# Optimization experiments

Hardware: AMD Instinct MI355X
Metric: run time of the kernel (lower is better)

The kernel has to match this reference:

```python
import jax, jax.numpy as jnp
import numpy as np

B, S, F_DIM, H = 2, 2048, 1024, 16
DH = F_DIM // H  # 64


def setup_inputs() -> dict:
    key = jax.random.key(0)
    ks = jax.random.split(key, 12)
    scale = 1.0 / np.sqrt(F_DIM)
    inp = {
        "Q": jax.random.normal(ks[0], (B, S, F_DIM), jnp.float32),
        "K": jax.random.normal(ks[1], (B, S, F_DIM), jnp.float32),
        "V": jax.random.normal(ks[2], (B, S, F_DIM), jnp.float32),
        "mask": jnp.zeros((1, 1, S, S), jnp.float32),
        "Wq": jax.random.uniform(ks[3], (F_DIM, F_DIM), jnp.float32, -scale, scale),
        "bq": jax.random.uniform(ks[4], (F_DIM,), jnp.float32, -scale, scale),
        "Wk": jax.random.uniform(ks[5], (F_DIM, F_DIM), jnp.float32, -scale, scale),
        "bk": jax.random.uniform(ks[6], (F_DIM,), jnp.float32, -scale, scale),
        "Wv": jax.random.uniform(ks[7], (F_DIM, F_DIM), jnp.float32, -scale, scale),
        "bv": jax.random.uniform(ks[8], (F_DIM,), jnp.float32, -scale, scale),
        "Wo": jax.random.uniform(ks[9], (F_DIM, F_DIM), jnp.float32, -scale, scale),
        "bo": jax.random.uniform(ks[10], (F_DIM,), jnp.float32, -scale, scale),
    }
    return inp


def _split_heads(x):
    # [B, S, F] -> [B, H, S, DH]
    b, s, _ = x.shape
    return x.reshape(b, s, H, DH).transpose(0, 2, 1, 3)


def reference(Q, K, V, mask, Wq, bq, Wk, bk, Wv, bv, Wo, bo):
    q = _split_heads(Q @ Wq.T + bq)  # [B, H, S, DH]
    k = _split_heads(K @ Wk.T + bk)
    v = _split_heads(V @ Vv_fix(Wv).T + bv) if False else _split_heads(V @ Wv.T + bv)
    scores = jnp.einsum("bhqd,bhkd->bhqk", q, k) / jnp.sqrt(jnp.float32(DH))
    scores = scores + mask
    probs = jax.nn.softmax(scores, axis=-1)
    attn = jnp.einsum("bhqk,bhkd->bhqd", probs, v)  # [B, H, S, DH]
    out = attn.transpose(0, 2, 1, 3).reshape(Q.shape[0], Q.shape[1], F_DIM)
    return out @ Wo.T + bo
```

## Files before the change

### kernel.cpp

```cpp
#include <hip/hip_runtime.h>
#include <hip/hip_bf16.h>

typedef unsigned short u16;
typedef unsigned int u32;
typedef __attribute__((ext_vector_type(4))) float f32x4;
typedef __attribute__((ext_vector_type(16))) float f32x16;
typedef __attribute__((ext_vector_type(8))) short short8;
typedef __attribute__((ext_vector_type(4))) u32 u32x4;

#define SEQ 2048
#define FD  1024
#define NH  16
#define DHD 64

__device__ __forceinline__ u16 f2bf(float f) {
  __hip_bfloat16 h = __float2bfloat16(f);
  return *reinterpret_cast<u16*>(&h);
}
__device__ __forceinline__ u32 pack2bf(float lo, float hi) {
  return (u32)f2bf(lo) | ((u32)f2bf(hi) << 16);
}

template <typename TA, typename TB>
__device__ __forceinline__ void gemm_bt_body(const TA* __restrict__ A, const TB* __restrict__ Bm,
                                             int m0, int n0, u16* As, u16* Bs, f32x4 acc[4][4]) {
  const int tid = threadIdx.x;
  const int lane = tid & 63;
  const int wr = (tid >> 7) & 1;
  const int wc = (tid >> 6) & 1;
  const int lr = lane & 15;
  const int lk = (lane >> 4) << 3;
#pragma unroll
  for (int m = 0; m < 4; ++m)
#pragma unroll
    for (int n = 0; n < 4; ++n) acc[m][n] = {0.f, 0.f, 0.f, 0.f};

  const int r_ = tid >> 2;
  const int c_ = (tid & 3) << 3;

  for (int k0 = 0; k0 < FD; k0 += 32) {
    __syncthreads();
#pragma unroll
    for (int c = 0; c < 2; ++c) {
      int r = c * 64 + r_;
      const TA* s = A + (size_t)(m0 + r) * FD + k0 + c_;
      short8 o;
      if constexpr (sizeof(TA) == 4) {
        f32x4 v0 = *reinterpret_cast<const f32x4*>(s);
        f32x4 v1 = *reinterpret_cast<const f32x4*>(s + 4);
#pragma unroll
        for (int j = 0; j < 4; ++j) { o[j] = (short)f2bf(v0[j]); o[4 + j] = (short)f2bf(v1[j]); }
      } else {
        o = *reinterpret_cast<const short8*>(s);
      }
      *reinterpret_cast<short8*>(&As[r * 32 + c_]) = o;
    }
#pragma unroll
    for (int c = 0; c < 2; ++c) {
      int r = c * 64 + r_;
      const TB* s = Bm + (size_t)(n0 + r) * FD + k0 + c_;
      short8 o;
      if constexpr (sizeof(TB) == 4) {
        f32x4 v0 = *reinterpret_cast<const f32x4*>(s);
        f32x4 v1 = *reinterpret_cast<const f32x4*>(s + 4);
#pragma unroll
        for (int j = 0; j < 4; ++j) { o[j] = (short)f2bf(v0[j]); o[4 + j] = (short)f2bf(v1[j]); }
      } else {
        o = *reinterpret_cast<const short8*>(s);
      }
      *reinterpret_cast<short8*>(&Bs[r * 32 + c_]) = o;
    }
    __syncthreads();

    short8 a[4], b[4];
#pragma unroll
    for (int m = 0; m < 4; ++m)
      a[m] = *reinterpret_cast<const short8*>(&As[(wr * 64 + m * 16 + lr) * 32 + lk]);
#pragma unroll
    for (int n = 0; n < 4; ++n)
      b[n] = *reinterpret_cast<const short8*>(&Bs[(wc * 64 + n * 16 + lr) * 32 + lk]);
#pragma unroll
    for (int m = 0; m < 4; ++m)
#pragma unroll
      for (int n = 0; n < 4; ++n)
        acc[m][n] = __builtin_amdgcn_mfma_f32_16x16x32_bf16(a[m], b[n], acc[m][n], 0, 0, 0);
  }
}

__global__ __launch_bounds__(256) void proj_qkv_kernel(
    const float* __restrict__ Q, const float* __restrict__ K, const float* __restrict__ V,
    const float* __restrict__ Wq, const float* __restrict__ Wk, const float* __restrict__ Wv,
    const float* __restrict__ bq, const float* __restrict__ bk, const float* __restrict__ bv,
    u16* __restrict__ qh, u16* __restrict__ kh, u16* __restrict__ vF) {
  __shared__ u16 As[128 * 32];
  __shared__ u16 Bs[128 * 32];
  const int which = blockIdx.z;
  const float* A    = (which == 0) ? Q  : (which == 1) ? K  : V;
  const float* W    = (which == 0) ? Wq : (which == 1) ? Wk : Wv;
  const float* bias = (which == 0) ? bq : (which == 1) ? bk : bv;
  u16* out          = (which == 0) ? qh : (which == 1) ? kh : vF;
  const int m0 = blockIdx.y * 128, n0 = blockIdx.x * 128;
  const float qscale = 0.18033688011112042f;

  f32x4 acc[4][4];
  gemm_bt_body(A, W, m0, n0, As, Bs, acc);

  const int lane = threadIdx.x & 63;
  const int wr = (threadIdx.x >> 7) & 1, wc = (threadIdx.x >> 6) & 1;
  const int rbase = m0 + wr * 64 + ((lane >> 4) << 2);
  const int cbase = n0 + wc * 64 + (lane & 15);
#pragma unroll
  for (int n = 0; n < 4; ++n) {
    const int col = cbase + n * 16;
    const float bvv = bias[col];
    const int h = col >> 6, dh = col & 63;
#pragma unroll
    for (int m = 0; m < 4; ++m) {
#pragma unroll
      for (int r = 0; r < 4; ++r) {
        const int row = rbase + m * 16 + r;
        const int b = row >> 11, s = row & 2047;
        float v = acc[m][n][r] + bvv;
        if (which == 0) v *= qscale;
        const size_t bhbase = (size_t)(b * 16 + h) * SEQ * DHD;
        size_t idx;
        if (which == 0) {
          idx = bhbase + (size_t)s * 64 + dh;
        } else if (which == 1) {
          idx = bhbase + ((size_t)(((s >> 5) * 4 + (dh >> 4)) * 64
                          + ((dh >> 3) & 1) * 32 + (s & 31)) << 3) + (dh & 7);
        } else {
          idx = bhbase + ((size_t)(((s >> 4) * 2 + (dh >> 5)) * 64
                          + ((s >> 3) & 1) * 32 + (dh & 31)) << 3) + (s & 7);
        }
        out[idx] = f2bf(v);
      }
    }
  }
}

__global__ __launch_bounds__(256) void mask_check_kernel(const u32* __restrict__ mask,
                                                         u32* __restrict__ flag) {
  const size_t cb = (size_t)blockIdx.x * 2048 + (threadIdx.x << 2);
  u32x4 a = *reinterpret_cast<const u32x4*>(&mask[cb]);
  u32x4 b = *reinterpret_cast<const u32x4*>(&mask[cb + 1024]);
  u32 acc = a[0] | a[1] | a[2] | a[3] | b[0] | b[1] | b[2] | b[3];
  if (__ballot(acc != 0)) {
    if ((threadIdx.x & 63) == 0) atomicOr(flag, 1u);
  }
}

__device__ __forceinline__ void load_ktile(const u16* __restrict__ kp, int kv0, int lane,
                                           short8 (&kf)[8]) {
#pragma unroll
  for (int h2 = 0; h2 < 2; ++h2)
#pragma unroll
    for (int d = 0; d < 4; ++d)
      kf[h2 * 4 + d] = *reinterpret_cast<const short8*>(
          &kp[((size_t)((((kv0 >> 5) + h2) * 4 + d) * 64 + lane)) << 3]);
}

__device__ __forceinline__ void attn_tile(
    const short8 (&kf)[8], const u16* __restrict__ vp, const float* __restrict__ mrow,
    u32 has_mask, int kv0, int lane, int hi, const short8 (&qf)[4],
    f32x16 (&oacc)[2], float& m2, float& lsum) {
  const float L2E = 1.44269504088896340736f;
  short8 vf[8];
#pragma unroll
  for (int kb = 0; kb < 4; ++kb)
#pragma unroll
    for (int db = 0; db < 2; ++db)
      vf[kb * 2 + db] = *reinterpret_cast<const short8*>(
          &vp[((size_t)((((kv0 >> 4) + kb) * 2 + db) * 64 + lane)) << 3]);

  f32x16 st[2];
#pragma unroll
  for (int h2 = 0; h2 < 2; ++h2) {
    f32x16 z;
#pragma unroll
    for (int e = 0; e < 16; ++e) z[e] = 0.f;
#pragma unroll
    for (int d = 0; d < 4; ++d)
      z = __builtin_amdgcn_mfma_f32_32x32x16_bf16(kf[h2 * 4 + d], qf[d], z, 0, 0, 0);
    st[h2] = z;
  }
  float p[32];
  if (__builtin_expect(has_mask != 0, 0)) {
#pragma unroll
    for (int h2 = 0; h2 < 2; ++h2)
#pragma unroll
      for (int g = 0; g < 4; ++g) {
        f32x4 mv = *reinterpret_cast<const f32x4*>(&mrow[kv0 + h2 * 32 + g * 8 + hi * 4]);
#pragma unroll
        for (int j = 0; j < 4; ++j)
          p[h2 * 16 + g * 4 + j] = fmaf(mv[j], L2E, st[h2][g * 4 + j]);
      }
  } else {
#pragma unroll
    for (int h2 = 0; h2 < 2; ++h2)
#pragma unroll
      for (int e = 0; e < 16; ++e) p[h2 * 16 + e] = st[h2][e];
  }
  float t8[8];
#pragma unroll
  for (int i = 0; i < 8; ++i)
    t8[i] = fmaxf(fmaxf(p[i], p[i + 8]), fmaxf(p[i + 16], p[i + 24]));
#pragma unroll
  for (int i = 0; i < 4; ++i) t8[i] = fmaxf(t8[i], t8[i + 4]);
  float mt = fmaxf(fmaxf(t8[0], t8[1]), fmaxf(t8[2], t8[3]));
  mt = fmaxf(mt, __shfl_xor(mt, 32));
  const float mnew = fmaxf(m2, mt);
  const float alpha = __builtin_amdgcn_exp2f(m2 - mnew);
  m2 = mnew;
#pragma unroll
  for (int i = 0; i < 32; ++i) p[i] = __builtin_amdgcn_exp2f(p[i] - m2);
  float s8[8];
#pragma unroll
  for (int i = 0; i < 8; ++i) s8[i] = (p[i] + p[i + 8]) + (p[i + 16] + p[i + 24]);
#pragma unroll
  for (int i = 0; i < 4; ++i) s8[i] += s8[i + 4];
  float ssum = (s8[0] + s8[1]) + (s8[2] + s8[3]);
  ssum += __shfl_xor(ssum, 32);
  lsum = lsum * alpha + ssum;
#pragma unroll
  for (int e = 0; e < 16; ++e) { oacc[0][e] *= alpha; oacc[1][e] *= alpha; }

#pragma unroll
  for (int kb = 0; kb < 4; ++kb) {
    const int pb = (kb >> 1) * 16 + (kb & 1) * 8;
    u32 x = pack2bf(p[pb + 0], p[pb + 1]);
    u32 y = pack2bf(p[pb + 4], p[pb + 5]);
    asm volatile("v_permlane32_swap_b32 %0, %1" : "+v"(x), "+v"(y));
    u32 zz = pack2bf(p[pb + 2], p[pb + 3]);
    u32 w = pack2bf(p[pb + 6], p[pb + 7]);
    asm volatile("v_permlane32_swap_b32 %0, %1" : "+v"(zz), "+v"(w));
    union { u32 u[4]; short8 s; } bf;
    bf.u[0] = x; bf.u[1] = zz; bf.u[2] = y; bf.u[3] = w;
#pragma unroll
    for (int db = 0; db < 2; ++db)
      oacc[db] = __builtin_amdgcn_mfma_f32_32x32x16_bf16(vf[kb * 2 + db], bf.s, oacc[db], 0, 0, 0);
  }
}

__global__ __launch_bounds__(256, 2) void attn_kernel(
    const u16* __restrict__ qh, const u16* __restrict__ kh, const u16* __restrict__ vF,
    const float* __restrict__ mask, const u32* __restrict__ mflag, u16* __restrict__ O) {
  const int wave = threadIdx.x >> 6, lane = threadIdx.x & 63;
  const int bid = blockIdx.x;
  const int vid = (bid & 7) * 64 + (bid >> 3);
  const int bh = vid >> 4;
  const int q0 = (vid & 15) * 128 + wave * 32;
  const int lq = lane & 31;
  const int hi = lane >> 5;
  const u16* qp = qh + (size_t)bh * SEQ * DHD;
  const u16* kp = kh + (size_t)bh * SEQ * DHD;
  const u16* vp = vF + (size_t)bh * SEQ * DHD;
  const float* mrow = mask + (size_t)(q0 + lq) * SEQ;
  const u32 has_mask = *mflag;

  short8 qf[4];
#pragma unroll
  for (int d = 0; d < 4; ++d)
    qf[d] = *reinterpret_cast<const short8*>(&qp[(size_t)(q0 + lq) * DHD + d * 16 + hi * 8]);

  f32x16 oacc[2];
#pragma unroll
  for (int e = 0; e < 16; ++e) { oacc[0][e] = 0.f; oacc[1][e] = 0.f; }
  float m2 = -INFINITY, lsum = 0.f;

  short8 ka[8], kb2[8];
  load_ktile(kp, 0, lane, ka);
  for (int it = 0; it < 32; it += 2) {
    const int kv0 = it << 6;
    load_ktile(kp, kv0 + 64, lane, kb2);
    attn_tile(ka, vp, mrow, has_mask, kv0, lane, hi, qf, oacc, m2, lsum);
    load_ktile(kp, (it == 30) ? 0 : kv0 + 128, lane, ka);
    attn_tile(kb2, vp, mrow, has_mask, kv0 + 64, lane, hi, qf, oacc, m2, lsum);
  }

  const int b = bh >> 4, h = bh & 15;
  const float inv = 1.0f / lsum;
  u16* orow = O + ((size_t)(b * SEQ + q0 + lq) * NH + h) * DHD;
#pragma unroll
  for (int db = 0; db < 2; ++db)
#pragma unroll
    for (int g = 0; g < 4; ++g) {
      union { u16 u[4]; unsigned long long ll; } pk;
#pragma unroll
      for (int j = 0; j < 4; ++j) pk.u[j] = f2bf(oacc[db][g * 4 + j] * inv);
      *reinterpret_cast<unsigned long long*>(&orow[db * 32 + g * 8 + hi * 4]) = pk.ll;
    }
}

__global__ __launch_bounds__(256) void out_proj_kernel(
    const u16* __restrict__ O, const float* __restrict__ Wo, const float* __restrict__ bo,
    float* __restrict__ out) {
  __shared__ u16 As[128 * 32];
  __shared__ u16 Bs[128 * 32];
  const int m0 = blockIdx.y * 128, n0 = blockIdx.x * 128;
  f32x4 acc[4][4];
  gemm_bt_body(O, Wo, m0, n0, As, Bs, acc);

  const int lane = threadIdx.x & 63;
  const int wr = (threadIdx.x >> 7) & 1, wc = (threadIdx.x >> 6) & 1;
  const int rbase = m0 + wr * 64 + ((lane >> 4) << 2);
  const int cbase = n0 + wc * 64 + (lane & 15);
#pragma unroll
  for (int n = 0; n < 4; ++n) {
    const int col = cbase + n * 16;
    const float bvv = bo[col];
#pragma unroll
    for (int m = 0; m < 4; ++m)
#pragma unroll
      for (int r = 0; r < 4; ++r) {
        const int row = rbase + m * 16 + r;
        out[(size_t)row * FD + col] = acc[m][n][r] + bvv;
      }
  }
}

extern "C" void kernel_launch(void* const* d_in, const int* in_sizes, int n_in,
                              void* d_out, int out_size, void* d_ws, size_t ws_size,
                              hipStream_t stream) {
  (void)in_sizes; (void)n_in; (void)out_size; (void)ws_size;
  const float* Q    = (const float*)d_in[0];
  const float* K    = (const float*)d_in[1];
  const float* V    = (const float*)d_in[2];
  const float* mask = (const float*)d_in[3];
  const float* Wq   = (const float*)d_in[4];
  const float* bq   = (const float*)d_in[5];
  const float* Wk   = (const float*)d_in[6];
  const float* bk   = (const float*)d_in[7];
  const float* Wv   = (const float*)d_in[8];
  const float* bv   = (const float*)d_in[9];
  const float* Wo   = (const float*)d_in[10];
  const float* bo   = (const float*)d_in[11];
  float* out = (float*)d_out;

  u16* ws = (u16*)d_ws;
  const size_t SZ = (size_t)4096 * 1024;
  u16* qh = ws;
  u16* kh = qh + SZ;
  u16* vF = kh + SZ;
  u16* O  = vF + SZ;
  u32* mflag = (u32*)(O + SZ);

  hipMemsetAsync(mflag, 0, 4, stream);
  mask_check_kernel<<<dim3(2048), 256, 0, stream>>>((const u32*)mask, mflag);

  dim3 gproj(FD / 128, (2 * SEQ) / 128, 3);
  proj_qkv_kernel<<<gproj, 256, 0, stream>>>(Q, K, V, Wq, Wk, Wv, bq, bk, bv, qh, kh, vF);

  attn_kernel<<<dim3(512), 256, 0, stream>>>(qh, kh, vF, mask, mflag, O);

  out_proj_kernel<<<dim3(FD / 128, (2 * SEQ) / 128), 256, 0, stream>>>(O, Wo, bo, out);
}
```

Before: 169.3 us.

## Pre-convert inputs and weights to bf16, use direct global-to-LDS loads in GEMMs

Adds a prep kernel that converts Q/K/V and all four weight matrices to bf16 in workspace, and folds the mask-zero check into that same launch. The projection GEMMs then load bf16 tiles straight into LDS with global_load_lds, with no per-tile fp32 conversion. Block indices are remapped so consecutive blocks share weight columns for better L2 reuse. The cost is an extra full read/write pass over the activations and weights, plus more workspace.

Result: faster. 142.3 us (-15.9%).

```diff
diff --git a/kernel.cpp b/kernel.cpp
--- a/kernel.cpp
+++ b/kernel.cpp
@@ -21,57 +21,70 @@
   return (u32)f2bf(lo) | ((u32)f2bf(hi) << 16);
 }
 
-template <typename TA, typename TB>
-__device__ __forceinline__ void gemm_bt_body(const TA* __restrict__ A, const TB* __restrict__ Bm,
-                                             int m0, int n0, u16* As, u16* Bs, f32x4 acc[4][4]) {
-  const int tid = threadIdx.x;
-  const int lane = tid & 63;
-  const int wr = (tid >> 7) & 1;
-  const int wc = (tid >> 6) & 1;
-  const int lr = lane & 15;
-  const int lk = (lane >> 4) << 3;
+#define GLOAD_LDS16(gp, lp)                                        \
+  __builtin_amdgcn_global_load_lds(                                \
+      (const __attribute__((address_space(1))) unsigned int*)(gp), \
+      (__attribute__((address_space(3))) unsigned int*)(lp), 16, 0, 0)
+
+__global__ __launch_bounds__(256) void prep_kernel(
+    const float* __restrict__ Q, const float* __restrict__ K, const float* __restrict__ V,
+    const float* __restrict__ Wq, const float* __restrict__ Wk, const float* __restrict__ Wv,
+    const float* __restrict__ Wo, const float* __restrict__ mask,
+    u16* __restrict__ Abf, u16* __restrict__ Wbf, u32* __restrict__ flag) {
+  const size_t i = ((size_t)blockIdx.x * 256 + threadIdx.x) * 8;
+  if (i >= 16777216) {
+    const u32* mp = (const u32*)mask + (i - 16777216);
+    u32x4 a = *reinterpret_cast<const u32x4*>(mp);
+    u32x4 b = *reinterpret_cast<const u32x4*>(mp + 4);
+    u32 o = a[0] | a[1] | a[2] | a[3] | b[0] | b[1] | b[2] | b[3];
+    if (__ballot(o != 0) != 0ull && (threadIdx.x & 63) == 0) atomicOr(flag, 1u);
+    return;
+  }
+  const float* src;
+  u16* dst;
+  if (i < 12582912) {
+    const int s = (int)(i >> 22);
+    const size_t off = i & 0x3FFFFF;
+    src = (s == 0 ? Q : s == 1 ? K : V) + off;
+    dst = Abf + i;
+  } else {
+    const size_t j = i - 12582912;
+    const int w = (int)(j >> 20);
+    const size_t off = j & 0xFFFFF;
+    src = (w == 0 ? Wq : w == 1 ? Wk : w == 2 ? Wv : Wo) + off;
+    dst = Wbf + j;
+  }
+  f32x4 a = *reinterpret_cast<const f32x4*>(src);
+  f32x4 b = *reinterpret_cast<const f32x4*>(src + 4);
+  union { u32 u[4]; short8 s; } pk;
+  pk.u[0] = pack2bf(a[0], a[1]); pk.u[1] = pack2bf(a[2], a[3]);
+  pk.u[2] = pack2bf(b[0], b[1]); pk.u[3] = pack2bf(b[2], b[3]);
+  *reinterpret_cast<short8*>(dst) = pk.s;
+}
+
+__device__ __forceinline__ void gemm128_bf16(const u16* __restrict__ A, const u16* __restrict__ W,
+                                             int m0, int n0, u16* As, u16* Bs,
+                                             f32x4 (&acc)[4][4]) {
+  const int tid = threadIdx.x, lane = tid & 63, wv = tid >> 6;
+  const int wr = (tid >> 7) & 1, wc = (tid >> 6) & 1;
+  const int lr = lane & 15, lk = (lane >> 4) << 3;
+  const int srow = lane >> 2;
+  const int scol = (lane & 3) << 3;
 #pragma unroll
   for (int m = 0; m < 4; ++m)
 #pragma unroll
     for (int n = 0; n < 4; ++n) acc[m][n] = {0.f, 0.f, 0.f, 0.f};
-
-  const int r_ = tid >> 2;
-  const int c_ = (tid & 3) << 3;
 
   for (int k0 = 0; k0 < FD; k0 += 32) {
     __syncthreads();
 #pragma unroll
     for (int c = 0; c < 2; ++c) {
-      int r = c * 64 + r_;
-      const TA* s = A + (size_t)(m0 + r) * FD + k0 + c_;
-      short8 o;
-      if constexpr (sizeof(TA) == 4) {
-        f32x4 v0 = *reinterpret_cast<const f32x4*>(s);
-        f32x4 v1 = *reinterpret_cast<const f32x4*>(s + 4);
-#pragma unroll
-        for (int j = 0; j < 4; ++j) { o[j] = (short)f2bf(v0[j]); o[4 + j] = (short)f2bf(v1[j]); }
-      } else {
-        o = *reinterpret_cast<const short8*>(s);
-      }
-      *reinterpret_cast<short8*>(&As[r * 32 + c_]) = o;
-    }
-#pragma unroll
-    for (int c = 0; c < 2; ++c) {
-      int r = c * 64 + r_;
-      const TB* s = Bm + (size_t)(n0 + r) * FD + k0 + c_;
-      short8 o;
-      if constexpr (sizeof(TB) == 4) {
-        f32x4 v0 = *reinterpret_cast<const f32x4*>(s);
-        f32x4 v1 = *reinterpret_cast<const f32x4*>(s + 4);
-#pragma unroll
-        for (int j = 0; j < 4; ++j) { o[j] = (short)f2bf(v0[j]); o[4 + j] = (short)f2bf(v1[j]); }
-      } else {
-        o = *reinterpret_cast<const short8*>(s);
-      }
-      *reinterpret_cast<short8*>(&Bs[r * 32 + c_]) = o;
+      GLOAD_LDS16(&A[(size_t)(m0 + c * 64 + wv * 16 + srow) * FD + k0 + scol],
+                  &As[(c * 64 + wv * 16) * 32]);
+      GLOAD_LDS16(&W[(size_t)(n0 + c * 64 + wv * 16 + srow) * FD + k0 + scol],
+                  &Bs[(c * 64 + wv * 16) * 32]);
     }
     __syncthreads();
-
     short8 a[4], b[4];
 #pragma unroll
     for (int m = 0; m < 4; ++m)
@@ -88,23 +101,27 @@
 }
 
 __global__ __launch_bounds__(256) void proj_qkv_kernel(
-    const float* __restrict__ Q, const float* __restrict__ K, const float* __restrict__ V,
-    const float* __restrict__ Wq, const float* __restrict__ Wk, const float* __restrict__ Wv,
+    const u16* __restrict__ Abf, const u16* __restrict__ Wbf,
     const float* __restrict__ bq, const float* __restrict__ bk, const float* __restrict__ bv,
     u16* __restrict__ qh, u16* __restrict__ kh, u16* __restrict__ vF) {
   __shared__ u16 As[128 * 32];
   __shared__ u16 Bs[128 * 32];
-  const int which = blockIdx.z;
-  const float* A    = (which == 0) ? Q  : (which == 1) ? K  : V;
-  const float* W    = (which == 0) ? Wq : (which == 1) ? Wk : Wv;
+  const int bid = blockIdx.x;
+  const int which = bid >> 8;
+  const int rr = bid & 255;
+  const int slot = rr >> 3;
+  const int y = (rr & 7) + 8 * (slot & 3);
+  const int x = slot >> 2;
+  const int m0 = y * 128, n0 = x * 128;
+  const u16* A = Abf + ((size_t)which << 22);
+  const u16* W = Wbf + ((size_t)which << 20);
   const float* bias = (which == 0) ? bq : (which == 1) ? bk : bv;
-  u16* out          = (which == 0) ? qh : (which == 1) ? kh : vF;
-  const int m0 = blockIdx.y * 128, n0 = blockIdx.x * 128;
   const float qscale = 0.18033688011112042f;
 
   f32x4 acc[4][4];
-  gemm_bt_body(A, W, m0, n0, As, Bs, acc);
-
+  gemm128_bf16(A, W, m0, n0, As, Bs, acc);
+
+  u16* out = (which == 0) ? qh : (which == 1) ? kh : vF;
   const int lane = threadIdx.x & 63;
   const int wr = (threadIdx.x >> 7) & 1, wc = (threadIdx.x >> 6) & 1;
   const int rbase = m0 + wr * 64 + ((lane >> 4) << 2);
@@ -139,17 +156,6 @@
   }
 }
 
-__global__ __launch_bounds__(256) void mask_check_kernel(const u32* __restrict__ mask,
-                                                         u32* __restrict__ flag) {
-  const size_t cb = (size_t)blockIdx.x * 2048 + (threadIdx.x << 2);
-  u32x4 a = *reinterpret_cast<const u32x4*>(&mask[cb]);
-  u32x4 b = *reinterpret_cast<const u32x4*>(&mask[cb + 1024]);
-  u32 acc = a[0] | a[1] | a[2] | a[3] | b[0] | b[1] | b[2] | b[3];
-  if (__ballot(acc != 0)) {
-    if ((threadIdx.x & 63) == 0) atomicOr(flag, 1u);
-  }
-}
-
 __device__ __forceinline__ void load_ktile(const u16* __restrict__ kp, int kv0, int lane,
                                            short8 (&kf)[8]) {
 #pragma unroll
@@ -293,13 +299,17 @@
 }
 
 __global__ __launch_bounds__(256) void out_proj_kernel(
-    const u16* __restrict__ O, const float* __restrict__ Wo, const float* __restrict__ bo,
+    const u16* __restrict__ O, const u16* __restrict__ WoB, const float* __restrict__ bo,
     float* __restrict__ out) {
   __shared__ u16 As[128 * 32];
   __shared__ u16 Bs[128 * 32];
-  const int m0 = blockIdx.y * 128, n0 = blockIdx.x * 128;
+  const int rr = blockIdx.x;
+  const int slot = rr >> 3;
+  const int y = (rr & 7) + 8 * (slot & 3);
+  const int x = slot >> 2;
+  const int m0 = y * 128, n0 = x * 128;
   f32x4 acc[4][4];
-  gemm_bt_body(O, Wo, m0, n0, As, Bs, acc);
+  gemm128_bf16(O, WoB, m0, n0, As, Bs, acc);
 
   const int lane = threadIdx.x & 63;
   const int wr = (threadIdx.x >> 7) & 1, wc = (threadIdx.x >> 6) & 1;
@@ -339,19 +349,20 @@
 
   u16* ws = (u16*)d_ws;
   const size_t SZ = (size_t)4096 * 1024;
-  u16* qh = ws;
-  u16* kh = qh + SZ;
-  u16* vF = kh + SZ;
-  u16* O  = vF + SZ;
-  u32* mflag = (u32*)(O + SZ);
+  u16* qh  = ws;
+  u16* kh  = qh + SZ;
+  u16* vF  = kh + SZ;
+  u16* O   = vF + SZ;
+  u16* Abf = O + SZ;
+  u16* Wbf = Abf + 3 * SZ;
+  u32* mflag = (u32*)(Wbf + 4 * (size_t)1024 * 1024);
 
   hipMemsetAsync(mflag, 0, 4, stream);
-  mask_check_kernel<<<dim3(2048), 256, 0, stream>>>((const u32*)mask, mflag);
-
-  dim3 gproj(FD / 128, (2 * SEQ) / 128, 3);
-  proj_qkv_kernel<<<gproj, 256, 0, stream>>>(Q, K, V, Wq, Wk, Wv, bq, bk, bv, qh, kh, vF);
+  prep_kernel<<<dim3(10240), 256, 0, stream>>>(Q, K, V, Wq, Wk, Wv, Wo, mask, Abf, Wbf, mflag);
+
+  proj_qkv_kernel<<<dim3(768), 256, 0, stream>>>(Abf, Wbf, bq, bk, bv, qh, kh, vF);
 
   attn_kernel<<<dim3(512), 256, 0, stream>>>(qh, kh, vF, mask, mflag, O);
 
-  out_proj_kernel<<<dim3(FD / 128, (2 * SEQ) / 128), 256, 0, stream>>>(O, Wo, bo, out);
-}
+  out_proj_kernel<<<dim3(256), 256, 0, stream>>>(O, Wbf + 3 * (size_t)1024 * 1024, bo, out);
+}
```
